# Kernel optimization log

Measured on AMD Instinct MI355X. Metric: run time of the kernel, lower is better.

## Reference

```python
import jax, jax.numpy as jnp
import numpy as np

EPS = 1e-6
K = 16
TEMP = 1.0
RES_SCALE = 0.5
CLAMP_MAX = 50.0


def _knn_indices(x, k):
    # x: (B,N,3) -> idx (B,N,k), self excluded; squared dist preserves ordering
    sq = jnp.sum(x * x, axis=-1)                      # (B,N)
    d2 = sq[:, :, None] + sq[:, None, :] - 2.0 * jnp.einsum('bnd,bmd->bnm', x, x)
    N = x.shape[1]
    eye = jnp.eye(N, dtype=bool)
    d2 = jnp.where(eye[None], jnp.inf, d2)
    _, idx = jax.lax.top_k(-d2, k)
    return idx


def _gather(t, idx):
    # t: (B,N,...), idx: (B,N,k) -> (B,N,k,...)
    return jax.vmap(lambda tb, ib: tb[ib])(t, idx)


def _vn_linear(v, W):
    return jnp.einsum('bncd,oc->bnod', v, W)


def _edge_mlp(s, W1, b1, W2, b2, W3, b3):
    h = jax.nn.silu(s @ W1.T + b1)
    h = jax.nn.silu(h @ W2.T + b2)
    return h @ W3.T + b3


def _vn_layer_norm(x, gamma, beta):
    norm = jnp.maximum(jnp.linalg.norm(x, axis=-1), EPS)      # (B,N,C)
    mean = jnp.mean(norm, axis=-1, keepdims=True)
    std = jnp.maximum(jnp.std(norm, axis=-1, keepdims=True, ddof=1), EPS)
    norm_scaled = (norm - mean) / std * gamma + beta
    return x / norm[..., None] * jnp.maximum(norm_scaled[..., None], EPS)


def _clamp_features(x, max_norm):
    n = jnp.maximum(jnp.linalg.norm(x, axis=-1, keepdims=True), EPS)
    scale = jnp.minimum(max_norm / n, 1.0)
    return x * scale


def setup_inputs() -> dict:
    key = jax.random.key(0)
    ks = jax.random.split(key, 12)
    B, N, C, Cout, H = 8, 2048, 128, 128, 32
    gain = 0.5
    lim = gain * np.sqrt(6.0 / (C + Cout))
    inp = {
        'x': jax.random.normal(ks[0], (B, N, 3), jnp.float32),
        'v': jax.random.normal(ks[1], (B, N, C, 3), jnp.float32),
        'Wq': jax.random.uniform(ks[2], (Cout, C), jnp.float32, -lim, lim),
        'Wk': jax.random.uniform(ks[3], (Cout, C), jnp.float32, -lim, lim),
        'Wu': jax.random.uniform(ks[4], (Cout, C), jnp.float32, -lim, lim),
        'W1': jax.random.normal(ks[5], (H, 4), jnp.float32) * 0.3,
        'b1': jnp.zeros((H,), jnp.float32),
        'W2': jax.random.normal(ks[6], (H, H), jnp.float32) * 0.15,
        'b2': jnp.zeros((H,), jnp.float32),
        'W3': jax.random.normal(ks[7], (1, H), jnp.float32) * 0.15,
        'b3': jnp.zeros((1,), jnp.float32),
        'gamma': jnp.ones((Cout,), jnp.float32),
        'beta': jnp.zeros((Cout,), jnp.float32),
    }
    return inp


def reference(x, v, Wq, Wk, Wu, W1, b1, W2, b2, W3, b3, gamma, beta):
    idx = _knn_indices(jax.lax.stop_gradient(x), K)           # (B,N,k)
    x_nbr = _gather(x, idx)                                    # (B,N,k,3)
    Q = _vn_linear(v, Wq)                                      # (B,N,Co,3)
    Kt = _vn_linear(v, Wk)
    U = _vn_linear(v, Wu)
    K_nbr = _gather(Kt, idx)                                   # (B,N,k,Co,3)
    U_nbr = _gather(U, idx)
    qn = jnp.mean(jnp.linalg.norm(Q, axis=-1), axis=-1, keepdims=True)   # (B,N,1)
    kn = jnp.mean(jnp.linalg.norm(Kt, axis=-1), axis=-1, keepdims=True)
    kn_nbr = _gather(kn, idx)                                  # (B,N,k,1)
    dot_nbr = jnp.mean(jnp.sum(Q[:, :, None] * K_nbr, axis=-1), axis=-1, keepdims=True)  # (B,N,k,1)
    dist = jnp.linalg.norm(x[:, :, None] - x_nbr, axis=-1, keepdims=True)                # (B,N,k,1)
    qn_exp = jnp.broadcast_to(qn[:, :, None], kn_nbr.shape)
    edge_s = jnp.concatenate([qn_exp, kn_nbr, dot_nbr, dist], axis=-1)   # (B,N,k,4)
    logits = jnp.clip(_edge_mlp(edge_s, W1, b1, W2, b2, W3, b3) / TEMP, -10.0, 10.0)
    attn = jax.nn.softmax(logits, axis=2)                      # (B,N,k,1)
    msg = jnp.sum(attn[..., None] * U_nbr, axis=2)             # (B,N,Co,3)
    out = Q + RES_SCALE * msg
    out = _vn_layer_norm(out, gamma, beta)
    out = _clamp_features(out, CLAMP_MAX)
    return out
```

## Files before the change

### kernel.cpp

```cpp
#include <hip/hip_runtime.h>
#include <math.h>

#define BB 8
#define NN 2048
#define CC 128
#define KNB 16
#define BN (BB*NN)
#define WPAD 136

#define EMPTYK 0xFFFFFFFFFFFFFFFFULL

typedef __attribute__((ext_vector_type(8))) short short8;
typedef __attribute__((ext_vector_type(4))) float floatx4;
typedef __attribute__((ext_vector_type(4), aligned(4))) float floatx4u;

__device__ __forceinline__ float silu_f(float x) {
  const float e = __builtin_amdgcn_exp2f(-1.442695040888963f * x);
  return x * __builtin_amdgcn_rcpf(1.0f + e);
}
__device__ __forceinline__ float fsqrt(float x) { return __builtin_amdgcn_sqrtf(x); }
__device__ __forceinline__ float frcp(float x)  { return __builtin_amdgcn_rcpf(x); }

__device__ __forceinline__ unsigned long long umin64(unsigned long long a, unsigned long long b) {
  return (b < a) ? b : a;
}

__device__ __forceinline__ unsigned short f2bf(float f) {
  unsigned u = __float_as_uint(f);
  unsigned r = u + 0x7FFFu + ((u >> 16) & 1u);
  return (unsigned short)(r >> 16);
}
__device__ __forceinline__ float bf2f(unsigned short s) {
  return __uint_as_float(((unsigned)s) << 16);
}

__device__ __forceinline__ float dot8(const float* __restrict__ w, const float* __restrict__ h) {
  const float4 a = *(const float4*)w;
  const float4 b = *(const float4*)(w + 4);
  float s = a.x*h[0];
  s = fmaf(a.y, h[1], s); s = fmaf(a.z, h[2], s); s = fmaf(a.w, h[3], s);
  s = fmaf(b.x, h[4], s); s = fmaf(b.y, h[5], s); s = fmaf(b.z, h[6], s);
  s = fmaf(b.w, h[7], s);
  return s;
}

__global__ __launch_bounds__(256) void knn_kernel(const float* __restrict__ x,
                                                  int* __restrict__ idx) {
  const int lane = threadIdx.x & 63;
  const int wave = threadIdx.x >> 6;
  const int bn = blockIdx.x * 4 + wave;
  const int b = bn >> 11;
  const int n = bn & (NN - 1);

  const float* xb = x + (size_t)b * NN * 3;
  const double xn0 = (double)xb[n*3+0], xn1 = (double)xb[n*3+1], xn2 = (double)xb[n*3+2];
  const double sqn = xn0*xn0 + xn1*xn1 + xn2*xn2;

  unsigned long long k[32];
  unsigned long long t0 = EMPTYK, t1 = EMPTYK, t2 = EMPTYK, t3 = EMPTYK;

  #pragma unroll
  for (int i = 0; i < 32; ++i) {
    const int m = i*64 + lane;
    const double a0 = (double)xb[m*3+0], a1 = (double)xb[m*3+1], a2 = (double)xb[m*3+2];
    const double sqm = a0*a0 + a1*a1 + a2*a2;
    const double dot = xn0*a0 + xn1*a1 + xn2*a2;
    const double d = sqn + sqm - 2.0*dot;
    unsigned long long kk =
        ((unsigned long long)__double_as_longlong(d) & ~2047ULL) | (unsigned long long)m;
    if (m == n) kk = 0x8000000000000000ULL | (unsigned long long)m;
    k[i] = kk;
    const bool l3 = kk < t3, l2 = kk < t2, l1 = kk < t1, l0 = kk < t0;
    t3 = l3 ? (l2 ? t2 : kk) : t3;
    t2 = l2 ? (l1 ? t1 : kk) : t2;
    t1 = l1 ? (l0 ? t0 : kk) : t1;
    t0 = l0 ? kk : t0;
  }

  int* op = idx + (size_t)bn * KNB;
  for (int t = 0; t < KNB; ++t) {
    unsigned long long g = t0;
    #pragma unroll
    for (int off = 32; off > 0; off >>= 1)
      g = umin64(g, (unsigned long long)__shfl_xor((unsigned long long)g, off, 64));

    if (lane == 0) op[t] = (int)(g & 2047ULL);

    const bool own = (t0 == g);
    t0 = own ? t1 : t0;
    t1 = own ? t2 : t1;
    t2 = own ? t3 : t2;
    t3 = own ? EMPTYK : t3;

    const bool need = (t0 == EMPTYK);
    if (__any(need)) {
      unsigned long long nm = EMPTYK;
      #pragma unroll
      for (int i = 0; i < 32; ++i) {
        const unsigned long long c = (k[i] > g) ? k[i] : EMPTYK;
        nm = umin64(nm, c);
      }
      t0 = need ? nm : t0;
    }
  }
}

__global__ __launch_bounds__(256) void wconv_kernel(
    const float* __restrict__ Wq, const float* __restrict__ Wk, const float* __restrict__ Wu,
    unsigned short* __restrict__ Whl)
{
  const int i = blockIdx.x*256 + threadIdx.x;
  const int mat = i >> 14, rem = i & 16383;
  const float* W = (mat == 0) ? Wq : ((mat == 1) ? Wk : Wu);
  const float f = W[rem];
  const unsigned short h = f2bf(f);
  const float r = f - bf2f(h);
  unsigned short* base = Whl + (size_t)mat * 2 * CC * CC;
  base[rem]           = h;
  base[CC*CC + rem]   = f2bf(r);
}

__global__ __launch_bounds__(256, 2) void vn_gemm_mfma(
    const float* __restrict__ v, const unsigned short* __restrict__ Whl,
    float* __restrict__ Q, float* __restrict__ Kt, float* __restrict__ U)
{
  __shared__ short Wh[CC][WPAD];
  __shared__ short Wl[CC][WPAD];

  const int tid  = threadIdx.x;
  const int lane = tid & 63;
  const int wave = tid >> 6;
  const int quad = lane >> 4;
  const int l15  = lane & 15;

  const int m = blockIdx.x*64 + wave*16 + l15;
  const int p = m / 3, d = m - 3*p;
  const float* vb = v + (size_t)p * (CC*3) + d;
  float areg[32];
  #pragma unroll
  for (int kc = 0; kc < 4; ++kc)
    #pragma unroll
    for (int j = 0; j < 8; ++j)
      areg[kc*8+j] = vb[(kc*32 + quad*8 + j)*3];

  short8 ah[4], al[4];
  #pragma unroll
  for (int kc = 0; kc < 4; ++kc)
    #pragma unroll
    for (int j = 0; j < 8; ++j) {
      const float f = areg[kc*8+j];
      unsigned short h = f2bf(f);
      float r = f - bf2f(h);
      ah[kc][j] = (short)h;
      al[kc][j] = (short)f2bf(r);
    }

  const int r0s = blockIdx.x*64 + wave*16 + quad*4;
  int pbase[4];
  #pragma unroll
  for (int reg = 0; reg < 4; ++reg) {
    const int r = r0s + reg;
    const int pp = r / 3;
    pbase[reg] = pp * (CC*3) + (r - 3*pp);
  }
  const int l153 = l15 * 3;

  for (int mat = 0; mat < 3; ++mat) {
    float* __restrict__ Out = (mat == 0) ? Q : ((mat == 1) ? Kt : U);
    const unsigned short* Wg = Whl + (size_t)mat * 2 * CC * CC;

    #pragma unroll
    for (int it = 0; it < 8; ++it) {
      const int i = it*256 + tid;
      const int o = i >> 4, c8 = (i & 15) * 8;
      *(short8*)&Wh[o][c8] = *(const short8*)&Wg[o*CC + c8];
      *(short8*)&Wl[o][c8] = *(const short8*)&Wg[CC*CC + o*CC + c8];
    }
    __syncthreads();

    floatx4 acc[8];
    #pragma unroll
    for (int ct = 0; ct < 8; ++ct) acc[ct] = (floatx4){0.f, 0.f, 0.f, 0.f};

    #pragma unroll
    for (int kc = 0; kc < 4; ++kc) {
      #pragma unroll
      for (int ct = 0; ct < 8; ++ct) {
        const int o = ct*16 + l15;
        const short8 bh = *(const short8*)&Wh[o][kc*32 + quad*8];
        const short8 bl = *(const short8*)&Wl[o][kc*32 + quad*8];
        acc[ct] = __builtin_amdgcn_mfma_f32_16x16x32_bf16(ah[kc], bh, acc[ct], 0, 0, 0);
        acc[ct] = __builtin_amdgcn_mfma_f32_16x16x32_bf16(al[kc], bh, acc[ct], 0, 0, 0);
        acc[ct] = __builtin_amdgcn_mfma_f32_16x16x32_bf16(ah[kc], bl, acc[ct], 0, 0, 0);
      }
    }
    __syncthreads();

    #pragma unroll
    for (int ct = 0; ct < 8; ++ct) {
      const int o3 = ct*48 + l153;
      #pragma unroll
      for (int reg = 0; reg < 4; ++reg)
        Out[pbase[reg] + o3] = acc[ct][reg];
    }
  }
}

__global__ __launch_bounds__(256) void kn_kernel(const float* __restrict__ Kt,
                                                 float* __restrict__ kn) {
  const int lane = threadIdx.x & 63;
  const int wave = threadIdx.x >> 6;
  const int bn = blockIdx.x * 4 + wave;
  const float* Kp = Kt + (size_t)bn * (CC*3) + lane*6;
  const floatx4u a = *(const floatx4u*)Kp;
  const float2 c = *(const float2*)(Kp+4);
  float s = fsqrt(a.x*a.x + a.y*a.y + a.z*a.z) + fsqrt(a.w*a.w + c.x*c.x + c.y*c.y);
  #pragma unroll
  for (int off = 1; off < 64; off <<= 1) s += __shfl_xor(s, off, 64);
  if (lane == 0) kn[bn] = s * (1.0f/128.0f);
}

__global__ __launch_bounds__(256) void attn_wave_kernel(
    const float* __restrict__ x, const int* __restrict__ idx,
    const float* __restrict__ Q, const float* __restrict__ Kt, const float* __restrict__ U,
    const float* __restrict__ kn,
    const float* __restrict__ W1, const float* __restrict__ b1,
    const float* __restrict__ W2, const float* __restrict__ b2,
    const float* __restrict__ W3, const float* __restrict__ b3,
    const float* __restrict__ gam, const float* __restrict__ bet,
    float* __restrict__ out)
{
  const int lane = threadIdx.x & 63;
  const int wv   = threadIdx.x >> 6;
  const int bn = ((blockIdx.x & 7) << 11) | (((blockIdx.x >> 3) << 2) | wv);
  const int b = bn >> 11;

  const float* Qp = Q + (size_t)bn * (CC*3) + lane*6;
  const floatx4u q0 = *(const floatx4u*)Qp;
  const float2 q1 = *(const float2*)(Qp+4);
  const float2 qa = make_float2(q0.x, q0.y);
  const float2 qb = make_float2(q0.z, q0.w);
  const float2 qc = make_float2(q1.x, q1.y);

  const int* ip = idx + (size_t)bn * KNB;
  int j[KNB];
  #pragma unroll
  for (int t = 0; t < KNB; ++t) j[t] = ip[t];

  const int kk = lane & 15;
  int jsel = j[0];
  #pragma unroll
  for (int t = 1; t < KNB; ++t) jsel = (kk == t) ? j[t] : jsel;

  const float xi0 = x[(size_t)bn*3+0], xi1 = x[(size_t)bn*3+1], xi2 = x[(size_t)bn*3+2];
  const float* xj = x + (size_t)(b*NN + jsel)*3;
  const float xj0 = xj[0], xj1 = xj[1], xj2 = xj[2];
  const float s1 = kn[(size_t)b*NN + jsel];

  float dpart[KNB];
  #pragma unroll
  for (int t = 0; t < KNB; ++t) {
    const float* Kp = Kt + (size_t)(b*NN + j[t]) * (CC*3) + lane*6;
    const floatx4u kv = *(const floatx4u*)Kp;
    const float2 kw = *(const float2*)(Kp+4);
    dpart[t] = qa.x*kv.x + qa.y*kv.y + qb.x*kv.z + qb.y*kv.w + qc.x*kw.x + qc.y*kw.y;
  }
  float qnp = fsqrt(qa.x*qa.x + qa.y*qa.y + qb.x*qb.x) + fsqrt(qb.y*qb.y + qc.x*qc.x + qc.y*qc.y);

  #pragma unroll
  for (int off = 1; off < 64; off <<= 1) qnp += __shfl_xor(qnp, off, 64);
  const float s0 = qnp * (1.0f/128.0f);

  float d8[8];
  {
    const bool hb = (lane & 1) != 0;
    #pragma unroll
    for (int t = 0; t < 8; ++t) {
      const float keep = hb ? dpart[2*t+1] : dpart[2*t];
      const float send = hb ? dpart[2*t]   : dpart[2*t+1];
      d8[t] = keep + __shfl_xor(send, 1, 64);
    }
  }
  float d4[4];
  {
    const bool hb = (lane & 2) != 0;
    #pragma unroll
    for (int t = 0; t < 4; ++t) {
      const float keep = hb ? d8[2*t+1] : d8[2*t];
      const float send = hb ? d8[2*t]   : d8[2*t+1];
      d4[t] = keep + __shfl_xor(send, 2, 64);
    }
  }
  float d2[2];
  {
    const bool hb = (lane & 4) != 0;
    #pragma unroll
    for (int t = 0; t < 2; ++t) {
      const float keep = hb ? d4[2*t+1] : d4[2*t];
      const float send = hb ? d4[2*t]   : d4[2*t+1];
      d2[t] = keep + __shfl_xor(send, 4, 64);
    }
  }
  float dsel;
  {
    const bool hb = (lane & 8) != 0;
    const float keep = hb ? d2[1] : d2[0];
    const float send = hb ? d2[0] : d2[1];
    dsel = keep + __shfl_xor(send, 8, 64);
  }
  dsel += __shfl_xor(dsel, 16, 64);
  dsel += __shfl_xor(dsel, 32, 64);

  const float dx = xi0 - xj0, dy = xi1 - xj1, dz = xi2 - xj2;
  const float s3 = fsqrt(dx*dx + dy*dy + dz*dz);
  const float s2 = dsel * (1.0f/128.0f);

  float u0[KNB], u1[KNB], u2[KNB], u3[KNB], u4[KNB], u5[KNB];
  #pragma unroll
  for (int t = 0; t < KNB; ++t) {
    const float* Up = U + (size_t)(b*NN + j[t]) * (CC*3) + lane*6;
    const floatx4u uv = *(const floatx4u*)Up;
    const float2 uw = *(const float2*)(Up+4);
    u0[t]=uv.x; u1[t]=uv.y; u2[t]=uv.z; u3[t]=uv.w; u4[t]=uw.x; u5[t]=uw.y;
  }

  const int g = lane >> 4;
  const int o0 = g*8, o1 = (g^1)*8, o2 = (g^2)*8, o3 = (g^3)*8;

  float h1o[8];
  {
    const float4 b1a = *(const float4*)(b1 + o0);
    const float4 b1b = *(const float4*)(b1 + o0 + 4);
    const float bb1[8] = {b1a.x,b1a.y,b1a.z,b1a.w,b1b.x,b1b.y,b1b.z,b1b.w};
    #pragma unroll
    for (int jj = 0; jj < 8; ++jj) {
      const float4 w = *(const float4*)(W1 + (o0 + jj)*4);
      float u = bb1[jj];
      u = fmaf(w.x, s0, u); u = fmaf(w.y, s1, u);
      u = fmaf(w.z, s2, u); u = fmaf(w.w, s3, u);
      h1o[jj] = silu_f(u);
    }
  }
  float hx16[8], hx32[8], hx48[8];
  #pragma unroll
  for (int jj = 0; jj < 8; ++jj) hx16[jj] = __shfl_xor(h1o[jj], 16, 64);
  #pragma unroll
  for (int jj = 0; jj < 8; ++jj) hx32[jj] = __shfl_xor(h1o[jj], 32, 64);
  #pragma unroll
  for (int jj = 0; jj < 8; ++jj) hx48[jj] = __shfl_xor(hx16[jj], 32, 64);

  float logit;
  {
    const float4 b2a = *(const float4*)(b2 + o0);
    const float4 b2b = *(const float4*)(b2 + o0 + 4);
    const float bb2[8] = {b2a.x,b2a.y,b2a.z,b2a.w,b2b.x,b2b.y,b2b.z,b2b.w};
    const float4 w3a = *(const float4*)(W3 + o0);
    const float4 w3b = *(const float4*)(W3 + o0 + 4);
    const float ww3[8] = {w3a.x,w3a.y,w3a.z,w3a.w,w3b.x,w3b.y,w3b.z,w3b.w};
    float lp = 0.f;
    #pragma unroll
    for (int hh = 0; hh < 8; ++hh) {
      const float* wr = W2 + (o0 + hh)*32;
      float a = bb2[hh];
      a += dot8(wr + o0, h1o);
      a += dot8(wr + o1, hx16);
      a += dot8(wr + o2, hx32);
      a += dot8(wr + o3, hx48);
      lp = fmaf(ww3[hh], silu_f(a), lp);
    }
    lp += __shfl_xor(lp, 16, 64);
    lp += __shfl_xor(lp, 32, 64);
    logit = lp + b3[0];
  }
  logit = fminf(fmaxf(logit, -10.0f), 10.0f);

  float mx = logit;
  #pragma unroll
  for (int off = 8; off > 0; off >>= 1) mx = fmaxf(mx, __shfl_xor(mx, off, 16));
  const float e = __builtin_amdgcn_exp2f(1.442695040888963f * (logit - mx));
  float ssum = e;
  #pragma unroll
  for (int off = 8; off > 0; off >>= 1) ssum += __shfl_xor(ssum, off, 16);
  const float w = e * frcp(ssum);

  float wk[KNB];
  #pragma unroll
  for (int t = 0; t < KNB; ++t) wk[t] = __shfl(w, t, 64);

  float m0=0.f,m1=0.f,m2=0.f,m3=0.f,m4=0.f,m5=0.f;
  #pragma unroll
  for (int t = 0; t < KNB; ++t) {
    const float ww = wk[t];
    m0 = fmaf(ww, u0[t], m0); m1 = fmaf(ww, u1[t], m1); m2 = fmaf(ww, u2[t], m2);
    m3 = fmaf(ww, u3[t], m3); m4 = fmaf(ww, u4[t], m4); m5 = fmaf(ww, u5[t], m5);
  }
  const float oa0 = qa.x + 0.5f*m0, oa1 = qa.y + 0.5f*m1, oa2 = qb.x + 0.5f*m2;
  const float ob0 = qb.y + 0.5f*m3, ob1 = qc.x + 0.5f*m4, ob2 = qc.y + 0.5f*m5;

  const float na = fmaxf(fsqrt(oa0*oa0 + oa1*oa1 + oa2*oa2), 1e-6f);
  const float nb = fmaxf(fsqrt(ob0*ob0 + ob1*ob1 + ob2*ob2), 1e-6f);
  float s = na + nb;
  #pragma unroll
  for (int off = 1; off < 64; off <<= 1) s += __shfl_xor(s, off, 64);
  const float mean = s * (1.0f/128.0f);
  const float dva = na - mean, dvb = nb - mean;
  float s2v = dva*dva + dvb*dvb;
  #pragma unroll
  for (int off = 1; off < 64; off <<= 1) s2v += __shfl_xor(s2v, off, 64);
  const float stdv = fmaxf(fsqrt(s2v * (1.0f/127.0f)), 1e-6f);
  const float rstd = frcp(stdv);

  const float2 gm = *(const float2*)(gam + lane*2);
  const float2 bt = *(const float2*)(bet + lane*2);
  const float nsa = (na - mean) * rstd * gm.x + bt.x;
  const float nsb = (nb - mean) * rstd * gm.y + bt.y;
  const float sca = fmaxf(nsa, 1e-6f) * frcp(na);
  const float scb = fmaxf(nsb, 1e-6f) * frcp(nb);
  float fa0 = oa0*sca, fa1 = oa1*sca, fa2 = oa2*sca;
  float fb0 = ob0*scb, fb1 = ob1*scb, fb2 = ob2*scb;
  const float n2a = fmaxf(fsqrt(fa0*fa0 + fa1*fa1 + fa2*fa2), 1e-6f);
  const float n2b = fmaxf(fsqrt(fb0*fb0 + fb1*fb1 + fb2*fb2), 1e-6f);
  const float c2a = fminf(50.0f * frcp(n2a), 1.0f);
  const float c2b = fminf(50.0f * frcp(n2b), 1.0f);

  float* op = out + (size_t)bn * (CC*3) + lane*6;
  floatx4u o4; o4.x = fa0*c2a; o4.y = fa1*c2a; o4.z = fa2*c2a; o4.w = fb0*c2b;
  *(floatx4u*)op = o4;
  *(float2*)(op+4) = make_float2(fb1*c2b, fb2*c2b);
}

extern "C" void kernel_launch(void* const* d_in, const int* in_sizes, int n_in,
                              void* d_out, int out_size, void* d_ws, size_t ws_size,
                              hipStream_t stream) {
  (void)in_sizes; (void)n_in; (void)out_size; (void)ws_size;
  const float* x   = (const float*)d_in[0];
  const float* v   = (const float*)d_in[1];
  const float* Wq  = (const float*)d_in[2];
  const float* Wk  = (const float*)d_in[3];
  const float* Wu  = (const float*)d_in[4];
  const float* W1  = (const float*)d_in[5];
  const float* b1  = (const float*)d_in[6];
  const float* W2  = (const float*)d_in[7];
  const float* b2  = (const float*)d_in[8];
  const float* W3  = (const float*)d_in[9];
  const float* b3  = (const float*)d_in[10];
  const float* gam = (const float*)d_in[11];
  const float* bet = (const float*)d_in[12];
  float* out = (float*)d_out;

  char* ws = (char*)d_ws;
  int*   idx = (int*)ws;
  float* Q   = (float*)(ws + (size_t)BN * KNB * 4);
  float* Kt  = Q  + (size_t)BN * CC * 3;
  float* U   = Kt + (size_t)BN * CC * 3;
  unsigned short* Whl = (unsigned short*)(U + (size_t)BN * CC * 3);
  float* kn  = (float*)((char*)Whl + (size_t)3 * 2 * CC * CC * 2);

  knn_kernel<<<BN/4, 256, 0, stream>>>(x, idx);
  wconv_kernel<<<192, 256, 0, stream>>>(Wq, Wk, Wu, Whl);
  vn_gemm_mfma<<<(BN*3)/64, 256, 0, stream>>>(v, Whl, Q, Kt, U);
  kn_kernel<<<BN/4, 256, 0, stream>>>(Kt, kn);
  attn_wave_kernel<<<BN/4, 256, 0, stream>>>(x, idx, Q, Kt, U, kn,
                                             W1, b1, W2, b2, W3, b3, gam, bet, out);
}
```

Baseline: 279.3 us.

## Split attention kernel, transpose Q/K/U to planar layout, precompute squared norms

Stores Q/K/U with each spatial component as a contiguous 128-channel plane instead of interleaved (c,d), so the neighbour gathers read coalesced float2 per plane. Splits the attention kernel into a logits kernel and a message/normalisation kernel that pass weights through a workspace array, which reduces register pressure in each. The GEMM reuses a single LDS buffer for the hi and lo weight halves to cut shared memory, and KNN precomputes squared norms and does the top-k reduction with 32-bit shuffles plus a ballot fast path. The cost is extra launches and extra global traffic for the weights and re-read of idx/Q.

Result: no change. 282.8 us (+1.3%).

```diff
diff --git a/kernel.cpp b/kernel.cpp
--- a/kernel.cpp
+++ b/kernel.cpp
@@ -6,7 +6,7 @@
 #define CC 128
 #define KNB 16
 #define BN (BB*NN)
-#define WPAD 136
+#define WPAD 132
 
 #define EMPTYK 0xFFFFFFFFFFFFFFFFULL
 
@@ -44,7 +44,15 @@
   return s;
 }
 
+__global__ __launch_bounds__(256) void sq_kernel(const float* __restrict__ x,
+                                                 double* __restrict__ sqd) {
+  const int i = blockIdx.x*256 + threadIdx.x;
+  const double a0 = (double)x[i*3+0], a1 = (double)x[i*3+1], a2 = (double)x[i*3+2];
+  sqd[i] = a0*a0 + a1*a1 + a2*a2;
+}
+
 __global__ __launch_bounds__(256) void knn_kernel(const float* __restrict__ x,
+                                                  const double* __restrict__ sqd,
                                                   int* __restrict__ idx) {
   const int lane = threadIdx.x & 63;
   const int wave = threadIdx.x >> 6;
@@ -53,8 +61,9 @@
   const int n = bn & (NN - 1);
 
   const float* xb = x + (size_t)b * NN * 3;
+  const double* sqb = sqd + (size_t)b * NN;
   const double xn0 = (double)xb[n*3+0], xn1 = (double)xb[n*3+1], xn2 = (double)xb[n*3+2];
-  const double sqn = xn0*xn0 + xn1*xn1 + xn2*xn2;
+  const double sqn = sqb[n];
 
   unsigned long long k[32];
   unsigned long long t0 = EMPTYK, t1 = EMPTYK, t2 = EMPTYK, t3 = EMPTYK;
@@ -63,7 +72,7 @@
   for (int i = 0; i < 32; ++i) {
     const int m = i*64 + lane;
     const double a0 = (double)xb[m*3+0], a1 = (double)xb[m*3+1], a2 = (double)xb[m*3+2];
-    const double sqm = a0*a0 + a1*a1 + a2*a2;
+    const double sqm = sqb[m];
     const double dot = xn0*a0 + xn1*a1 + xn2*a2;
     const double d = sqn + sqm - 2.0*dot;
     unsigned long long kk =
@@ -79,14 +88,33 @@
 
   int* op = idx + (size_t)bn * KNB;
   for (int t = 0; t < KNB; ++t) {
-    unsigned long long g = t0;
-    #pragma unroll
-    for (int off = 32; off > 0; off >>= 1)
-      g = umin64(g, (unsigned long long)__shfl_xor((unsigned long long)g, off, 64));
-
-    if (lane == 0) op[t] = (int)(g & 2047ULL);
-
-    const bool own = (t0 == g);
+    const unsigned h0 = (unsigned)(t0 >> 32);
+    const unsigned l0w = (unsigned)t0;
+    unsigned hm = h0;
+    #pragma unroll
+    for (int off = 32; off > 0; off >>= 1) {
+      const unsigned o = (unsigned)__shfl_xor((int)hm, off, 64);
+      hm = (o < hm) ? o : hm;
+    }
+    const bool tied = (h0 == hm);
+    const unsigned long long bal = __ballot(tied);
+    unsigned lm;
+    if (__builtin_popcountll(bal) == 1) {
+      const int owner = __builtin_ctzll(bal);
+      lm = (unsigned)__shfl((int)l0w, owner, 64);
+    } else {
+      lm = tied ? l0w : 0xFFFFFFFFu;
+      #pragma unroll
+      for (int off = 32; off > 0; off >>= 1) {
+        const unsigned o = (unsigned)__shfl_xor((int)lm, off, 64);
+        lm = (o < lm) ? o : lm;
+      }
+    }
+    const unsigned long long g = ((unsigned long long)hm << 32) | (unsigned long long)lm;
+
+    if (lane == 0) op[t] = (int)(lm & 2047u);
+
+    const bool own = tied && (l0w == lm);
     t0 = own ? t1 : t0;
     t1 = own ? t2 : t1;
     t2 = own ? t3 : t2;
@@ -124,8 +152,7 @@
     const float* __restrict__ v, const unsigned short* __restrict__ Whl,
     float* __restrict__ Q, float* __restrict__ Kt, float* __restrict__ U)
 {
-  __shared__ short Wh[CC][WPAD];
-  __shared__ short Wl[CC][WPAD];
+  __shared__ short Wlds[CC][WPAD];
 
   const int tid  = threadIdx.x;
   const int lane = tid & 63;
@@ -161,36 +188,47 @@
   for (int reg = 0; reg < 4; ++reg) {
     const int r = r0s + reg;
     const int pp = r / 3;
-    pbase[reg] = pp * (CC*3) + (r - 3*pp);
-  }
-  const int l153 = l15 * 3;
+    pbase[reg] = pp * (CC*3) + (r - 3*pp) * CC;
+  }
 
   for (int mat = 0; mat < 3; ++mat) {
     float* __restrict__ Out = (mat == 0) ? Q : ((mat == 1) ? Kt : U);
     const unsigned short* Wg = Whl + (size_t)mat * 2 * CC * CC;
 
+    floatx4 acc[8];
+    #pragma unroll
+    for (int ct = 0; ct < 8; ++ct) acc[ct] = (floatx4){0.f, 0.f, 0.f, 0.f};
+
     #pragma unroll
     for (int it = 0; it < 8; ++it) {
       const int i = it*256 + tid;
       const int o = i >> 4, c8 = (i & 15) * 8;
-      *(short8*)&Wh[o][c8] = *(const short8*)&Wg[o*CC + c8];
-      *(short8*)&Wl[o][c8] = *(const short8*)&Wg[CC*CC + o*CC + c8];
+      *(short8*)&Wlds[o][c8] = *(const short8*)&Wg[o*CC + c8];
     }
     __syncthreads();
-
-    floatx4 acc[8];
-    #pragma unroll
-    for (int ct = 0; ct < 8; ++ct) acc[ct] = (floatx4){0.f, 0.f, 0.f, 0.f};
-
     #pragma unroll
     for (int kc = 0; kc < 4; ++kc) {
       #pragma unroll
       for (int ct = 0; ct < 8; ++ct) {
-        const int o = ct*16 + l15;
-        const short8 bh = *(const short8*)&Wh[o][kc*32 + quad*8];
-        const short8 bl = *(const short8*)&Wl[o][kc*32 + quad*8];
+        const short8 bh = *(const short8*)&Wlds[ct*16 + l15][kc*32 + quad*8];
         acc[ct] = __builtin_amdgcn_mfma_f32_16x16x32_bf16(ah[kc], bh, acc[ct], 0, 0, 0);
         acc[ct] = __builtin_amdgcn_mfma_f32_16x16x32_bf16(al[kc], bh, acc[ct], 0, 0, 0);
+      }
+    }
+    __syncthreads();
+
+    #pragma unroll
+    for (int it = 0; it < 8; ++it) {
+      const int i = it*256 + tid;
+      const int o = i >> 4, c8 = (i & 15) * 8;
+      *(short8*)&Wlds[o][c8] = *(const short8*)&Wg[CC*CC + o*CC + c8];
+    }
+    __syncthreads();
+    #pragma unroll
+    for (int kc = 0; kc < 4; ++kc) {
+      #pragma unroll
+      for (int ct = 0; ct < 8; ++ct) {
+        const short8 bl = *(const short8*)&Wlds[ct*16 + l15][kc*32 + quad*8];
         acc[ct] = __builtin_amdgcn_mfma_f32_16x16x32_bf16(ah[kc], bl, acc[ct], 0, 0, 0);
       }
     }
@@ -198,10 +236,10 @@
 
     #pragma unroll
     for (int ct = 0; ct < 8; ++ct) {
-      const int o3 = ct*48 + l153;
+      const int o = ct*16 + l15;
       #pragma unroll
       for (int reg = 0; reg < 4; ++reg)
-        Out[pbase[reg] + o3] = acc[ct][reg];
+        Out[pbase[reg] + o] = acc[ct][reg];
     }
   }
 }
@@ -211,36 +249,35 @@
   const int lane = threadIdx.x & 63;
   const int wave = threadIdx.x >> 6;
   const int bn = blockIdx.x * 4 + wave;
-  const float* Kp = Kt + (size_t)bn * (CC*3) + lane*6;
-  const floatx4u a = *(const floatx4u*)Kp;
-  const float2 c = *(const float2*)(Kp+4);
-  float s = fsqrt(a.x*a.x + a.y*a.y + a.z*a.z) + fsqrt(a.w*a.w + c.x*c.x + c.y*c.y);
+  const float* Kp = Kt + (size_t)bn * (CC*3) + 2*lane;
+  const float2 kd0 = *(const float2*)Kp;
+  const float2 kd1 = *(const float2*)(Kp + CC);
+  const float2 kd2 = *(const float2*)(Kp + 2*CC);
+  float s = fsqrt(kd0.x*kd0.x + kd1.x*kd1.x + kd2.x*kd2.x)
+          + fsqrt(kd0.y*kd0.y + kd1.y*kd1.y + kd2.y*kd2.y);
   #pragma unroll
   for (int off = 1; off < 64; off <<= 1) s += __shfl_xor(s, off, 64);
   if (lane == 0) kn[bn] = s * (1.0f/128.0f);
 }
 
-__global__ __launch_bounds__(256) void attn_wave_kernel(
+__global__ __launch_bounds__(256) void attn_logits_kernel(
     const float* __restrict__ x, const int* __restrict__ idx,
-    const float* __restrict__ Q, const float* __restrict__ Kt, const float* __restrict__ U,
+    const float* __restrict__ Q, const float* __restrict__ Kt,
     const float* __restrict__ kn,
     const float* __restrict__ W1, const float* __restrict__ b1,
     const float* __restrict__ W2, const float* __restrict__ b2,
     const float* __restrict__ W3, const float* __restrict__ b3,
-    const float* __restrict__ gam, const float* __restrict__ bet,
-    float* __restrict__ out)
+    float* __restrict__ warr)
 {
   const int lane = threadIdx.x & 63;
   const int wv   = threadIdx.x >> 6;
   const int bn = ((blockIdx.x & 7) << 11) | (((blockIdx.x >> 3) << 2) | wv);
   const int b = bn >> 11;
 
-  const float* Qp = Q + (size_t)bn * (CC*3) + lane*6;
-  const floatx4u q0 = *(const floatx4u*)Qp;
-  const float2 q1 = *(const float2*)(Qp+4);
-  const float2 qa = make_float2(q0.x, q0.y);
-  const float2 qb = make_float2(q0.z, q0.w);
-  const float2 qc = make_float2(q1.x, q1.y);
+  const float* Qp = Q + (size_t)bn * (CC*3) + 2*lane;
+  const float2 qd0 = *(const float2*)Qp;
+  const float2 qd1 = *(const float2*)(Qp + CC);
+  const float2 qd2 = *(const float2*)(Qp + 2*CC);
 
   const int* ip = idx + (size_t)bn * KNB;
   int j[KNB];
@@ -260,12 +297,15 @@
   float dpart[KNB];
   #pragma unroll
   for (int t = 0; t < KNB; ++t) {
-    const float* Kp = Kt + (size_t)(b*NN + j[t]) * (CC*3) + lane*6;
-    const floatx4u kv = *(const floatx4u*)Kp;
-    const float2 kw = *(const float2*)(Kp+4);
-    dpart[t] = qa.x*kv.x + qa.y*kv.y + qb.x*kv.z + qb.y*kv.w + qc.x*kw.x + qc.y*kw.y;
-  }
-  float qnp = fsqrt(qa.x*qa.x + qa.y*qa.y + qb.x*qb.x) + fsqrt(qb.y*qb.y + qc.x*qc.x + qc.y*qc.y);
+    const float* Kp = Kt + (size_t)(b*NN + j[t]) * (CC*3) + 2*lane;
+    const float2 kd0 = *(const float2*)Kp;
+    const float2 kd1 = *(const float2*)(Kp + CC);
+    const float2 kd2 = *(const float2*)(Kp + 2*CC);
+    dpart[t] = qd0.x*kd0.x + qd1.x*kd1.x + qd2.x*kd2.x
+             + qd0.y*kd0.y + qd1.y*kd1.y + qd2.y*kd2.y;
+  }
+  float qnp = fsqrt(qd0.x*qd0.x + qd1.x*qd1.x + qd2.x*qd2.x)
+            + fsqrt(qd0.y*qd0.y + qd1.y*qd1.y + qd2.y*qd2.y);
 
   #pragma unroll
   for (int off = 1; off < 64; off <<= 1) qnp += __shfl_xor(qnp, off, 64);
@@ -314,15 +354,6 @@
   const float dx = xi0 - xj0, dy = xi1 - xj1, dz = xi2 - xj2;
   const float s3 = fsqrt(dx*dx + dy*dy + dz*dz);
   const float s2 = dsel * (1.0f/128.0f);
-
-  float u0[KNB], u1[KNB], u2[KNB], u3[KNB], u4[KNB], u5[KNB];
-  #pragma unroll
-  for (int t = 0; t < KNB; ++t) {
-    const float* Up = U + (size_t)(b*NN + j[t]) * (CC*3) + lane*6;
-    const floatx4u uv = *(const floatx4u*)Up;
-    const float2 uw = *(const float2*)(Up+4);
-    u0[t]=uv.x; u1[t]=uv.y; u2[t]=uv.z; u3[t]=uv.w; u4[t]=uw.x; u5[t]=uw.y;
-  }
 
   const int g = lane >> 4;
   const int o0 = g*8, o1 = (g^1)*8, o2 = (g^2)*8, o3 = (g^3)*8;
@@ -383,19 +414,48 @@
   for (int off = 8; off > 0; off >>= 1) ssum += __shfl_xor(ssum, off, 16);
   const float w = e * frcp(ssum);
 
+  if (lane < KNB) warr[(size_t)bn * KNB + lane] = w;
+}
+
+__global__ __launch_bounds__(256) void attn_msg_kernel(
+    const int* __restrict__ idx, const float* __restrict__ Q,
+    const float* __restrict__ U, const float* __restrict__ warr,
+    const float* __restrict__ gam, const float* __restrict__ bet,
+    float* __restrict__ out)
+{
+  const int lane = threadIdx.x & 63;
+  const int wv   = threadIdx.x >> 6;
+  const int bn = ((blockIdx.x & 7) << 11) | (((blockIdx.x >> 3) << 2) | wv);
+  const int b = bn >> 11;
+
+  const float* Qp = Q + (size_t)bn * (CC*3) + 2*lane;
+  const float2 qd0 = *(const float2*)Qp;
+  const float2 qd1 = *(const float2*)(Qp + CC);
+  const float2 qd2 = *(const float2*)(Qp + 2*CC);
+
+  const int* ip = idx + (size_t)bn * KNB;
+  int j[KNB];
+  #pragma unroll
+  for (int t = 0; t < KNB; ++t) j[t] = ip[t];
+
+  const float* wp = warr + (size_t)bn * KNB;
   float wk[KNB];
   #pragma unroll
-  for (int t = 0; t < KNB; ++t) wk[t] = __shfl(w, t, 64);
+  for (int t = 0; t < KNB; ++t) wk[t] = wp[t];
 
   float m0=0.f,m1=0.f,m2=0.f,m3=0.f,m4=0.f,m5=0.f;
   #pragma unroll
   for (int t = 0; t < KNB; ++t) {
+    const float* Up = U + (size_t)(b*NN + j[t]) * (CC*3) + 2*lane;
+    const float2 ud0 = *(const float2*)Up;
+    const float2 ud1 = *(const float2*)(Up + CC);
+    const float2 ud2 = *(const float2*)(Up + 2*CC);
     const float ww = wk[t];
-    m0 = fmaf(ww, u0[t], m0); m1 = fmaf(ww, u1[t], m1); m2 = fmaf(ww, u2[t], m2);
-    m3 = fmaf(ww, u3[t], m3); m4 = fmaf(ww, u4[t], m4); m5 = fmaf(ww, u5[t], m5);
-  }
-  const float oa0 = qa.x + 0.5f*m0, oa1 = qa.y + 0.5f*m1, oa2 = qb.x + 0.5f*m2;
-  const float ob0 = qb.y + 0.5f*m3, ob1 = qc.x + 0.5f*m4, ob2 = qc.y + 0.5f*m5;
+    m0 = fmaf(ww, ud0.x, m0); m1 = fmaf(ww, ud1.x, m1); m2 = fmaf(ww, ud2.x, m2);
+    m3 = fmaf(ww, ud0.y, m3); m4 = fmaf(ww, ud1.y, m4); m5 = fmaf(ww, ud2.y, m5);
+  }
+  const float oa0 = qd0.x + 0.5f*m0, oa1 = qd1.x + 0.5f*m1, oa2 = qd2.x + 0.5f*m2;
+  const float ob0 = qd0.y + 0.5f*m3, ob1 = qd1.y + 0.5f*m4, ob2 = qd2.y + 0.5f*m5;
 
   const float na = fmaxf(fsqrt(oa0*oa0 + oa1*oa1 + oa2*oa2), 1e-6f);
   const float nb = fmaxf(fsqrt(ob0*ob0 + ob1*ob1 + ob2*ob2), 1e-6f);
@@ -454,12 +514,16 @@
   float* Kt  = Q  + (size_t)BN * CC * 3;
   float* U   = Kt + (size_t)BN * CC * 3;
   unsigned short* Whl = (unsigned short*)(U + (size_t)BN * CC * 3);
-  float* kn  = (float*)((char*)Whl + (size_t)3 * 2 * CC * CC * 2);
-
-  knn_kernel<<<BN/4, 256, 0, stream>>>(x, idx);
+  float* warr = (float*)((char*)Whl + (size_t)3 * 2 * CC * CC * 2);
+  double* sqd = (double*)(warr + (size_t)BN * KNB);
+  float*  kn  = (float*)(sqd + (size_t)BN);
+
+  sq_kernel<<<BN/256, 256, 0, stream>>>(x, sqd);
+  knn_kernel<<<BN/4, 256, 0, stream>>>(x, sqd, idx);
   wconv_kernel<<<192, 256, 0, stream>>>(Wq, Wk, Wu, Whl);
   vn_gemm_mfma<<<(BN*3)/64, 256, 0, stream>>>(v, Whl, Q, Kt, U);
   kn_kernel<<<BN/4, 256, 0, stream>>>(Kt, kn);
-  attn_wave_kernel<<<BN/4, 256, 0, stream>>>(x, idx, Q, Kt, U, kn,
-                                             W1, b1, W2, b2, W3, b3, gam, bet, out);
-}
+  attn_logits_kernel<<<BN/4, 256, 0, stream>>>(x, idx, Q, Kt, kn,
+                                               W1, b1, W2, b2, W3, b3, warr);
+  attn_msg_kernel<<<BN/4, 256, 0, stream>>>(idx, Q, U, warr, gam, bet, out);
+}
```
